# Kernel optimization log

Measured on AMD Instinct MI355X. Metric: run time of the kernel, lower is better.

The kernel has to match this reference:

```python
import jax, jax.numpy as jnp
import numpy as np

TEMPERATURE = 0.2

def setup_inputs() -> dict:
    key = jax.random.key(0)
    k1, k2 = jax.random.split(key)
    projected = jax.random.normal(k1, (2048, 2, 256), dtype=jnp.float32)
    predicted = jax.random.normal(k2, (2048, 4, 256), dtype=jnp.float32)
    return {"projected": projected, "predicted": predicted}

def _l2norm(x, eps=1e-12):
    n = jnp.linalg.norm(x, axis=-1, keepdims=True)
    return x / jnp.maximum(n, eps)

def reference(projected, predicted):
    # projected: [B, Vg, D], predicted: [B, Vt, D], Vt >= Vg.
    # Single-process: all_gather is identity, rank=0 -> labels = arange(B).
    B, Vg, D = projected.shape
    Vt = predicted.shape[1]
    Vl = Vt - Vg
    p = _l2norm(projected)
    q = _l2norm(predicted)
    # All pairwise similarity matrices at once: [Vg, Vt, B, B]
    logits = jnp.einsum('bid,cjd->ijbc', p, q) / TEMPERATURE
    lse = jax.nn.logsumexpr if False else jax.scipy.special.logsumexp(logits, axis=-1)  # [Vg, Vt, B]
    diag = jnp.diagonal(logits, axis1=-2, axis2=-1)                                    # [Vg, Vt, B]
    L = jnp.mean(lse - diag, axis=-1)  # per-pair CE loss, shape [Vg, Vt]
    # global terms: i != ii, both in [0, Vg)
    global_sum = jnp.sum(L[:, :Vg] * (1.0 - jnp.eye(Vg, dtype=L.dtype)))
    num_global_terms = Vg * (Vg - 1)
    global_loss = global_sum / num_global_terms if num_global_terms > 0 else jnp.float32(0.0)
    # local terms: faithful to source -> predicted columns 0..Vl-1 (not offset)
    num_local_terms = Vg * Vl
    local_sum = jnp.sum(L[:, :Vl]) if Vl > 0 else jnp.float32(0.0)
    local_loss = local_sum / num_local_terms if num_local_terms > 0 else jnp.float32(0.0)
    num_terms = num_global_terms + num_local_terms
    total = (global_sum + local_sum) / num_terms
    return (total, global_loss, local_loss)
```

## Files before the change

### kernel.cpp

```cpp
#include <hip/hip_runtime.h>
#include <hip/hip_bf16.h>
#include <stdint.h>

#define TB 2048
#define TD 256

typedef __attribute__((ext_vector_type(8)))  short        bf16x8;
typedef __attribute__((ext_vector_type(16))) float        f32x16;

#define SQRT5 2.23606797749979f

__global__ __launch_bounds__(256) void nnclr_prep(const float* __restrict__ proj,
                                                  const float* __restrict__ pred,
                                                  unsigned short* __restrict__ pq2) {
    const int grp = blockIdx.x;
    const int v   = blockIdx.y;
    const int t   = threadIdx.x;

    __shared__ float rowbuf[32][260];
    __shared__ float scales[32];

    float x[32];
    #pragma unroll
    for (int m = 0; m < 32; ++m) {
        const int b = grp * 32 + m;
        const float* src = (v < 2) ? proj + ((size_t)b * 2 + v) * TD
                                   : pred + ((size_t)b * 4 + (v - 2)) * TD;
        x[m] = src[t];
    }
    #pragma unroll
    for (int m = 0; m < 32; ++m) rowbuf[m][t] = x[m];
    __syncthreads();

    {
        const int row = t >> 3, l8 = t & 7;
        float ss = 0.f;
        #pragma unroll
        for (int n = 0; n < 32; ++n) { const float y = rowbuf[row][l8 + 8 * n]; ss += y * y; }
        ss += __shfl_xor(ss, 1, 64);
        ss += __shfl_xor(ss, 2, 64);
        ss += __shfl_xor(ss, 4, 64);
        if (l8 == 0) scales[row] = SQRT5 / fmaxf(sqrtf(ss), 1e-12f);
    }
    __syncthreads();

    unsigned short* dst = pq2 + ((size_t)(v * 64 + grp) * 8192);
    const int col = t >> 3, e = t & 7;
    const float sc = scales[col];
    #pragma unroll
    for (int m = 0; m < 32; ++m) {
        const float y = rowbuf[col][m * 8 + e] * sc;
        const unsigned int bits = __float_as_uint(y);
        dst[m * 256 + t] = (unsigned short)((bits + 0x7FFFu + ((bits >> 16) & 1u)) >> 16);
    }
}

__global__ __launch_bounds__(256, 2) void nnclr_main(const unsigned short* __restrict__ pq2,
                                                     float* __restrict__ sPart,
                                                     float* __restrict__ dPart)
{
    const int rb = blockIdx.x, ch = blockIdx.y, j = blockIdx.z;
    const int tid = threadIdx.x, lane = tid & 63, wave = tid >> 6;
    const int cl = lane & 31, hk = lane >> 5;
    const int b0 = rb * 32;

    const bf16x8* P = (const bf16x8*)pq2;
    bf16x8 aF0[16], aF1[16];
    #pragma unroll
    for (int ks = 0; ks < 16; ++ks) {
        const int g = 2 * ks + hk;
        aF0[ks] = P[((0 * 64 + rb) * 32 + g) * 32 + cl];
        aF1[ks] = P[((1 * 64 + rb) * 32 + g) * 32 + cl];
    }

    float sAcc0[16], sAcc1[16];
    #pragma unroll
    for (int r = 0; r < 16; ++r) { sAcc0[r] = 0.f; sAcc1[r] = 0.f; }
    float d0 = 0.f, d1 = 0.f;
    const int  rDiag    = (cl & 3) + 4 * (cl >> 3);
    const bool laneDiag = (((cl >> 2) & 1) == hk);

    const bf16x8* Bbase = P + (size_t)(2 + j) * 64 * 32 * 32;
    const int cg0 = ch * 16 + wave * 4;

    bf16x8 bq[4];
    #pragma unroll
    for (int k = 0; k < 4; ++k) bq[k] = Bbase[(cg0 * 32 + 2 * k + hk) * 32 + cl];

    #pragma unroll
    for (int cgl = 0; cgl < 4; ++cgl) {
        const int cgAbs = cg0 + cgl;
        f32x16 acc0, acc1;
        #pragma unroll
        for (int r = 0; r < 16; ++r) { acc0[r] = 0.f; acc1[r] = 0.f; }
        #pragma unroll
        for (int ks = 0; ks < 16; ++ks) {
            const bf16x8 b = bq[ks & 3];
            if (ks < 12)          bq[ks & 3] = Bbase[(cgAbs * 32 + 2 * (ks + 4) + hk) * 32 + cl];
            else if (cgl < 3)     bq[ks & 3] = Bbase[((cgAbs + 1) * 32 + 2 * (ks - 12) + hk) * 32 + cl];
            acc0 = __builtin_amdgcn_mfma_f32_32x32x16_bf16(aF0[ks], b, acc0, 0, 0, 0);
            acc1 = __builtin_amdgcn_mfma_f32_32x32x16_bf16(aF1[ks], b, acc1, 0, 0, 0);
        }
        const bool diagCG = (cgAbs == rb);
        #pragma unroll
        for (int r = 0; r < 16; ++r) {
            const float v0 = acc0[r], v1 = acc1[r];
            sAcc0[r] += __expf(v0 - 5.0f);
            sAcc1[r] += __expf(v1 - 5.0f);
            if (diagCG) {
                const bool m = laneDiag && (r == rDiag);
                d0 += m ? v0 : 0.f;
                d1 += m ? v1 : 0.f;
            }
        }
    }

    #pragma unroll
    for (int r = 0; r < 16; ++r) {
        float s0 = sAcc0[r], s1 = sAcc1[r];
        #pragma unroll
        for (int msk = 1; msk < 32; msk <<= 1) {
            s0 += __shfl_xor(s0, msk, 64);
            s1 += __shfl_xor(s1, msk, 64);
        }
        sAcc0[r] = s0; sAcc1[r] = s1;
    }

    __shared__ float sArr[2][4][32];
    __shared__ float dArr[2][4][32];
    if (cl == 0) {
        #pragma unroll
        for (int r = 0; r < 16; ++r) {
            const int rowl = (r & 3) + 8 * (r >> 2) + 4 * hk;
            sArr[0][wave][rowl] = sAcc0[r];
            sArr[1][wave][rowl] = sAcc1[r];
        }
    }
    if (laneDiag) { dArr[0][wave][cl] = d0; dArr[1][wave][cl] = d1; }
    __syncthreads();
    if (tid < 64) {
        const int i = tid >> 5, row = tid & 31;
        float s = 0.f, d = 0.f;
        #pragma unroll
        for (int w = 0; w < 4; ++w) { s += sArr[i][w][row]; d += dArr[i][w][row]; }
        const int pair = i * 2 + j;
        const int b = b0 + row;
        sPart[((size_t)pair * TB + b) * 4 + ch] = s;
        dPart[((size_t)pair * TB + b) * 4 + ch] = d;
    }
}

__global__ __launch_bounds__(1024) void nnclr_final(const float* __restrict__ sPart,
                                                    const float* __restrict__ dPart,
                                                    float* __restrict__ out) {
    const int tid = threadIdx.x;
    float acc[4] = {0.f, 0.f, 0.f, 0.f};
    #pragma unroll
    for (int k = 0; k < 8; ++k) {
        const int row = tid + k * 1024;
        float s = 0.f, d = 0.f;
        #pragma unroll
        for (int c = 0; c < 4; ++c) { s += sPart[row * 4 + c]; d += dPart[row * 4 + c]; }
        acc[k >> 1] += 5.0f + logf(s) - d;
    }
    __shared__ float red[16][4];
    const int lane = tid & 63, wave = tid >> 6;
    #pragma unroll
    for (int p = 0; p < 4; ++p) {
        #pragma unroll
        for (int m = 1; m < 64; m <<= 1) acc[p] += __shfl_xor(acc[p], m, 64);
    }
    if (lane == 0) {
        #pragma unroll
        for (int p = 0; p < 4; ++p) red[wave][p] = acc[p];
    }
    __syncthreads();
    if (tid == 0) {
        float L[4];
        #pragma unroll
        for (int p = 0; p < 4; ++p) {
            float a = 0.f;
            for (int w = 0; w < 16; ++w) a += red[w][p];
            L[p] = a / (float)TB;
        }
        const float gs = L[1] + L[2];
        const float ls = L[0] + L[1] + L[2] + L[3];
        out[0] = (gs + ls) / 6.0f;
        out[1] = gs * 0.5f;
        out[2] = ls * 0.25f;
    }
}

extern "C" void kernel_launch(void* const* d_in, const int* in_sizes, int n_in,
                              void* d_out, int out_size, void* d_ws, size_t ws_size,
                              hipStream_t stream) {
    const float* projected = (const float*)d_in[0];
    const float* predicted = (const float*)d_in[1];

    unsigned short* pq2 = (unsigned short*)d_ws;
    float* sPart = (float*)((char*)d_ws + 4u * 1024u * 1024u);
    float* dPart = sPart + (size_t)4 * TB * 4;
    float* out = (float*)d_out;

    dim3 gprep(64, 4);
    nnclr_prep<<<gprep, 256, 0, stream>>>(projected, predicted, pq2);
    dim3 gmain(64, 4, 2);
    nnclr_main<<<gmain, 256, 0, stream>>>(pq2, sPart, dPart);
    nnclr_final<<<1, 1024, 0, stream>>>(sPart, dPart, out);
}
```

Before: 31.59 us.

## Deepen B prefetch to 8 stages and split final reduction across blocks

Raises the register prefetch depth for B fragments in the main MFMA loop from 4 to 8 k-steps so more global loads are in flight ahead of use. It also replaces the single-block final reduction with a 32-block kernel that uses vectorized float4 loads, followed by a tiny one-wave kernel that combines the partial sums. This spreads the reduction over many CUs but adds an extra kernel launch, and the larger prefetch buffer raises register pressure.

```diff
diff --git a/kernel.cpp b/kernel.cpp
--- a/kernel.cpp
+++ b/kernel.cpp
@@ -83,25 +83,25 @@
     const bf16x8* Bbase = P + (size_t)(2 + j) * 64 * 32 * 32;
     const int cg0 = ch * 16 + wave * 4;
 
-    bf16x8 bq[4];
-    #pragma unroll
-    for (int k = 0; k < 4; ++k) bq[k] = Bbase[(cg0 * 32 + 2 * k + hk) * 32 + cl];
+    bf16x8 bq[8];
+    #pragma unroll
+    for (int k = 0; k < 8; ++k) bq[k] = Bbase[(cg0 * 32 + 2 * k + hk) * 32 + cl];
 
     #pragma unroll
     for (int cgl = 0; cgl < 4; ++cgl) {
-        const int cgAbs = cg0 + cgl;
+        const int cg = cg0 + cgl;
         f32x16 acc0, acc1;
         #pragma unroll
         for (int r = 0; r < 16; ++r) { acc0[r] = 0.f; acc1[r] = 0.f; }
         #pragma unroll
         for (int ks = 0; ks < 16; ++ks) {
-            const bf16x8 b = bq[ks & 3];
-            if (ks < 12)          bq[ks & 3] = Bbase[(cgAbs * 32 + 2 * (ks + 4) + hk) * 32 + cl];
-            else if (cgl < 3)     bq[ks & 3] = Bbase[((cgAbs + 1) * 32 + 2 * (ks - 12) + hk) * 32 + cl];
+            const bf16x8 b = bq[ks & 7];
+            if (ks < 8)        bq[ks & 7] = Bbase[(cg * 32 + 2 * (ks + 8) + hk) * 32 + cl];
+            else if (cgl < 3)  bq[ks & 7] = Bbase[((cg + 1) * 32 + 2 * (ks - 8) + hk) * 32 + cl];
             acc0 = __builtin_amdgcn_mfma_f32_32x32x16_bf16(aF0[ks], b, acc0, 0, 0, 0);
             acc1 = __builtin_amdgcn_mfma_f32_32x32x16_bf16(aF1[ks], b, acc1, 0, 0, 0);
         }
-        const bool diagCG = (cgAbs == rb);
+        const bool diagCG = (cg == rb);
         #pragma unroll
         for (int r = 0; r < 16; ++r) {
             const float v0 = acc0[r], v1 = acc1[r];
@@ -150,41 +150,39 @@
     }
 }
 
-__global__ __launch_bounds__(1024) void nnclr_final(const float* __restrict__ sPart,
+__global__ __launch_bounds__(256) void nnclr_final1(const float* __restrict__ sPart,
                                                     const float* __restrict__ dPart,
-                                                    float* __restrict__ out) {
+                                                    float* __restrict__ Lpart) {
     const int tid = threadIdx.x;
-    float acc[4] = {0.f, 0.f, 0.f, 0.f};
-    #pragma unroll
-    for (int k = 0; k < 8; ++k) {
-        const int row = tid + k * 1024;
-        float s = 0.f, d = 0.f;
-        #pragma unroll
-        for (int c = 0; c < 4; ++c) { s += sPart[row * 4 + c]; d += dPart[row * 4 + c]; }
-        acc[k >> 1] += 5.0f + logf(s) - d;
-    }
-    __shared__ float red[16][4];
+    const int item = blockIdx.x * 256 + tid;
+    const float4 sv = ((const float4*)sPart)[item];
+    const float4 dv = ((const float4*)dPart)[item];
+    const float s = (sv.x + sv.y) + (sv.z + sv.w);
+    const float d = (dv.x + dv.y) + (dv.z + dv.w);
+    float L = 5.0f + logf(s) - d;
+    #pragma unroll
+    for (int m = 1; m < 64; m <<= 1) L += __shfl_xor(L, m, 64);
+    __shared__ float wsum[4];
     const int lane = tid & 63, wave = tid >> 6;
-    #pragma unroll
-    for (int p = 0; p < 4; ++p) {
-        #pragma unroll
-        for (int m = 1; m < 64; m <<= 1) acc[p] += __shfl_xor(acc[p], m, 64);
-    }
-    if (lane == 0) {
-        #pragma unroll
-        for (int p = 0; p < 4; ++p) red[wave][p] = acc[p];
-    }
-    __syncthreads();
-    if (tid == 0) {
-        float L[4];
-        #pragma unroll
-        for (int p = 0; p < 4; ++p) {
-            float a = 0.f;
-            for (int w = 0; w < 16; ++w) a += red[w][p];
-            L[p] = a / (float)TB;
-        }
-        const float gs = L[1] + L[2];
-        const float ls = L[0] + L[1] + L[2] + L[3];
+    if (lane == 0) wsum[wave] = L;
+    __syncthreads();
+    if (tid == 0) Lpart[blockIdx.x] = (wsum[0] + wsum[1]) + (wsum[2] + wsum[3]);
+}
+
+__global__ __launch_bounds__(64) void nnclr_final2(const float* __restrict__ Lpart,
+                                                   float* __restrict__ out) {
+    const int t = threadIdx.x;
+    float v = (t < 32) ? Lpart[t] : 0.f;
+    v += __shfl_xor(v, 1, 64);
+    v += __shfl_xor(v, 2, 64);
+    v += __shfl_xor(v, 4, 64);
+    const float L0 = __shfl(v, 0, 64)  * (1.0f / TB);
+    const float L1 = __shfl(v, 8, 64)  * (1.0f / TB);
+    const float L2 = __shfl(v, 16, 64) * (1.0f / TB);
+    const float L3 = __shfl(v, 24, 64) * (1.0f / TB);
+    if (t == 0) {
+        const float gs = L1 + L2;
+        const float ls = L0 + L1 + L2 + L3;
         out[0] = (gs + ls) / 6.0f;
         out[1] = gs * 0.5f;
         out[2] = ls * 0.25f;
@@ -200,11 +198,13 @@
     unsigned short* pq2 = (unsigned short*)d_ws;
     float* sPart = (float*)((char*)d_ws + 4u * 1024u * 1024u);
     float* dPart = sPart + (size_t)4 * TB * 4;
+    float* Lpart = dPart + (size_t)4 * TB * 4;
     float* out = (float*)d_out;
 
     dim3 gprep(64, 4);
     nnclr_prep<<<gprep, 256, 0, stream>>>(projected, predicted, pq2);
     dim3 gmain(64, 4, 2);
     nnclr_main<<<gmain, 256, 0, stream>>>(pq2, sPart, dPart);
-    nnclr_final<<<1, 1024, 0, stream>>>(sPart, dPart, out);
-}
+    nnclr_final1<<<32, 256, 0, stream>>>(sPart, dPart, Lpart);
+    nnclr_final2<<<1, 64, 0, stream>>>(Lpart, out);
+}
```

Measured after the change: 30.11 us. -4.7%, faster.
